# Performance work log

Hardware: AMD Instinct MI355X
Metric: run time of the kernel (lower is better)

## Reference

```python
import jax, jax.numpy as jnp
import numpy as np

B, L, D, H = 4, 2048, 1024, 16
NEG = 1e7


def pos_encodings(length, d_model, dtype):
    d_half = d_model // 2
    pos = jnp.arange(length, dtype=dtype)
    freqs = jnp.arange(d_half, dtype=dtype)
    periods = 1.0 / (10000.0 ** (freqs / d_half))
    ang = pos[:, None] * periods[None, :]          # [L, D/2]
    # interleave: even cols = sin, odd cols = cos
    return jnp.stack([jnp.sin(ang), jnp.cos(ang)], axis=-1).reshape(length, d_model)


def setup_inputs() -> dict:
    key = jax.random.key(0)
    ks = jax.random.split(key, 12)
    s = 1.0 / np.sqrt(D)
    return {
        "q": jax.random.normal(ks[0], (B, L, D), jnp.float32),
        "k": jax.random.normal(ks[1], (B, L, D), jnp.float32),
        "v": jax.random.normal(ks[2], (B, L, D), jnp.float32),
        "padding": jnp.zeros((B, L), dtype=bool),
        "Wq": jax.random.normal(ks[3], (D, D), jnp.float32) * s,
        "bq": jax.random.normal(ks[4], (D,), jnp.float32) * s,
        "Wk": jax.random.normal(ks[5], (D, D), jnp.float32) * s,
        "bk": jax.random.normal(ks[6], (D,), jnp.float32) * s,
        "Wv": jax.random.normal(ks[7], (D, D), jnp.float32) * s,
        "bv": jax.random.normal(ks[8], (D,), jnp.float32) * s,
        "Wo": jax.random.normal(ks[9], (D, D), jnp.float32) * s,
        "bo": jax.random.normal(ks[10], (D,), jnp.float32) * s,
    }


def reference(q, k, v, padding, Wq, bq, Wk, bk, Wv, bv, Wo, bo):
    dtype = q.dtype
    d_head = D // H
    pe = pos_encodings(L, D, dtype)                # cache_index = 0

    qp = (q + pe) @ Wq + bq                        # [B, L, D]
    kp = (k + pe) @ Wk + bk
    vp = v @ Wv + bv

    # ... l (h d) -> ... h l d
    def split_heads(x):
        return x.reshape(B, L, H, d_head).transpose(0, 2, 1, 3)

    qh, kh, vh = split_heads(qp), split_heads(kp), split_heads(vp)

    scores = jnp.einsum('bhqd,bhkd->bhqk', qh, kh) * (d_head ** -0.5)

    causal = jnp.triu(jnp.ones((L, L), dtype=bool), k=1)       # [L, L]
    mask = padding[:, None, None, :] | causal                  # [B, 1, L, L]
    scores = scores - mask.astype(scores.dtype) * NEG

    out = jnp.einsum('bhqk,bhkd->bhqd', jax.nn.softmax(scores, axis=-1), vh)
    out = out.transpose(0, 2, 1, 3).reshape(B, L, D)           # ... h l d -> ... l (h d)
    return out @ Wo + bo
```

## Files before the change

### kernel.cpp

```cpp
#include <hip/hip_runtime.h>
#include <hip/hip_bf16.h>


typedef __bf16 bf16_t;
typedef bf16_t bf16x8 __attribute__((ext_vector_type(8)));
typedef bf16_t bf16x4 __attribute__((ext_vector_type(4)));
typedef float  f32x4  __attribute__((ext_vector_type(4)));

#define MFMA_16x16x32(a, b, c) __builtin_amdgcn_mfma_f32_16x16x32_bf16((a), (b), (c), 0, 0, 0)

constexpr int Lc = 2048, Dc = 1024;
constexpr int Mc = 8192;
#define QSCALE 0.18033688011112042f

__device__ __forceinline__ void gload16(const void* g, void* l) {
  __builtin_amdgcn_global_load_lds(
      (const __attribute__((address_space(1))) void*)g,
      (__attribute__((address_space(3))) void*)l, 16, 0, 0);
}

template <bool DO_V>
__global__ __launch_bounds__(256)
void qkv_prep_kernel(const float* __restrict__ q, const float* __restrict__ k,
                     const float* __restrict__ v, bf16_t* __restrict__ Aq,
                     bf16_t* __restrict__ Ak, bf16_t* __restrict__ Av) {
  int id  = blockIdx.x * 256 + threadIdx.x;
  int row = id >> 7;
  int c   = (id & 127) * 8;
  int pos = row & (Lc - 1);
  float period = __expf(-(float)(c >> 1) * 0.017988946039015984f);
  const float ratio = 0.98217189f;
  float pe8[8];
#pragma unroll
  for (int j = 0; j < 4; ++j) {
    float rev = ((float)pos * period) * 0.15915494309189535f;
    float rf = rev - floorf(rev);
    pe8[2 * j]     = __builtin_amdgcn_sinf(rf);
    pe8[2 * j + 1] = __builtin_amdgcn_cosf(rf);
    period *= ratio;
  }
  size_t off = (size_t)row * Dc + c;
  f32x4 q0 = *(const f32x4*)&q[off], q1 = *(const f32x4*)&q[off + 4];
  f32x4 k0 = *(const f32x4*)&k[off], k1 = *(const f32x4*)&k[off + 4];
  bf16x8 aq, ak;
#pragma unroll
  for (int e = 0; e < 4; ++e) {
    aq[e]     = (bf16_t)(q0[e] + pe8[e]);
    aq[4 + e] = (bf16_t)(q1[e] + pe8[4 + e]);
    ak[e]     = (bf16_t)(k0[e] + pe8[e]);
    ak[4 + e] = (bf16_t)(k1[e] + pe8[4 + e]);
  }
  *(bf16x8*)&Aq[off] = aq;
  *(bf16x8*)&Ak[off] = ak;
  if (DO_V) {
    f32x4 v0 = *(const f32x4*)&v[off], v1 = *(const f32x4*)&v[off + 4];
    bf16x8 av;
#pragma unroll
    for (int e = 0; e < 4; ++e) { av[e] = (bf16_t)v0[e]; av[4 + e] = (bf16_t)v1[e]; }
    *(bf16x8*)&Av[off] = av;
  }
}

__device__ __forceinline__ void w_prep_body(const float* W, bf16_t* Wt, int tid, int blk) {
  __shared__ float tile[64][65];
  int k0 = (blk >> 4) * 64, n0 = (blk & 15) * 64;
  int tc = tid & 63, tr = tid >> 6;
#pragma unroll
  for (int j = 0; j < 16; ++j) {
    int r = j * 4 + tr;
    tile[r][tc] = W[(size_t)(k0 + r) * Dc + n0 + tc];
  }
  __syncthreads();
#pragma unroll
  for (int j = 0; j < 16; ++j) {
    int r = j * 4 + tr;
    Wt[(size_t)(n0 + r) * Dc + k0 + tc] = (bf16_t)tile[tc][r];
  }
}

__global__ __launch_bounds__(256)
void w_prep_kernel(const float* __restrict__ W, bf16_t* __restrict__ Wt) {
  w_prep_body(W, Wt, threadIdx.x, blockIdx.x);
}

__global__ __launch_bounds__(256)
void w_prep4_kernel(const float* __restrict__ W0, const float* __restrict__ W1,
                    const float* __restrict__ W2, const float* __restrict__ W3,
                    bf16_t* __restrict__ Wt) {
  int sel = blockIdx.x >> 8;
  const float* W = (sel == 0) ? W0 : (sel == 1) ? W1 : (sel == 2) ? W2 : W3;
  w_prep_body(W, Wt + (size_t)sel * Dc * Dc, threadIdx.x, blockIdx.x & 255);
}

template <bool TRANSOUT, typename OutT, int SEGS>
__global__ __launch_bounds__(512, 4)
void gemm_db_kernel(const bf16_t* __restrict__ A0, const bf16_t* __restrict__ A1,
                    const bf16_t* __restrict__ W0, const bf16_t* __restrict__ W1,
                    const float* __restrict__ b0, const float* __restrict__ b1,
                    OutT* __restrict__ C0, OutT* __restrict__ C1,
                    float s0, float s1) {
  constexpr int K = 1024, N = 1024, LDS_T = 136;
  __shared__ bf16_t smem[32768];
  int bid = blockIdx.x;
  int seg = (SEGS == 2) ? (bid >> 9) : 0;
  bid &= 511;
  const bf16_t* A    = seg ? A1 : A0;
  const bf16_t* Wt   = seg ? W1 : W0;
  const float*  bias = seg ? b1 : b0;
  OutT*         C    = seg ? C1 : C0;
  float scale        = seg ? s1 : s0;
  int xcd = bid & 7, slot = bid >> 3;
  int m0 = (xcd * 8 + (slot >> 3)) * 128;
  int n0 = (slot & 7) * 128;
  int t = threadIdx.x, lane = t & 63, w = t >> 6;
  int l16 = lane & 15, lq = lane >> 4;
  int wm = (w >> 1) * 32, wn = (w & 1) * 64;
  int srow = lane >> 3;
  int scol = ((lane & 7) ^ srow) << 3;
  int swz = l16 & 7;
  f32x4 acc[2][4] = {};

  auto STAGE = [&](int c, int k0) {
    bf16_t* Ash = &smem[c * 16384];
    bf16_t* Bsh = Ash + 8192;
#pragma unroll
    for (int j = 0; j < 2; ++j) {
      int r8 = (w * 2 + j) * 8;
      gload16(&A[(size_t)(m0 + r8 + srow) * K + k0 + scol], &Ash[r8 * 64]);
      gload16(&Wt[(size_t)(n0 + r8 + srow) * K + k0 + scol], &Bsh[r8 * 64]);
    }
  };

  STAGE(0, 0);
  int c = 0;
#pragma unroll 1
  for (int ti = 0; ti < 16; ++ti) {
    if (ti < 15) {
      STAGE(c ^ 1, (ti + 1) * 64);
      asm volatile("s_waitcnt vmcnt(4)" ::: "memory");
    } else {
      asm volatile("s_waitcnt vmcnt(0)" ::: "memory");
    }
    __builtin_amdgcn_s_barrier();
    const bf16_t* Ash = &smem[c * 16384];
    const bf16_t* Bsh = Ash + 8192;
#pragma unroll
    for (int ks = 0; ks < 2; ++ks) {
      bf16x8 af[2], bfr[4];
#pragma unroll
      for (int mt = 0; mt < 2; ++mt)
        af[mt] = *(const bf16x8*)&Ash[(wm + mt * 16 + l16) * 64 + (((ks * 4 + lq) ^ swz) << 3)];
#pragma unroll
      for (int nt = 0; nt < 4; ++nt)
        bfr[nt] = *(const bf16x8*)&Bsh[(wn + nt * 16 + l16) * 64 + (((ks * 4 + lq) ^ swz) << 3)];
#pragma unroll
      for (int mt = 0; mt < 2; ++mt)
#pragma unroll
        for (int nt = 0; nt < 4; ++nt)
          acc[mt][nt] = MFMA_16x16x32(af[mt], bfr[nt], acc[mt][nt]);
    }
    __builtin_amdgcn_s_barrier();
    c ^= 1;
  }

  if (TRANSOUT) {
    bf16_t* sT = smem;
#pragma unroll
    for (int nt = 0; nt < 4; ++nt) {
      float bv = bias[n0 + wn + nt * 16 + l16];
#pragma unroll
      for (int mt = 0; mt < 2; ++mt) {
        bf16x4 p4;
#pragma unroll
        for (int r = 0; r < 4; ++r) p4[r] = (bf16_t)(acc[mt][nt][r] + bv);
        *(bf16x4*)&sT[(wn + nt * 16 + l16) * LDS_T + wm + mt * 16 + lq * 4] = p4;
      }
    }
    __syncthreads();
    int b = m0 >> 11, kp0 = m0 & (Lc - 1);
#pragma unroll
    for (int i = 0; i < 4; ++i) {
      int cidx = t + i * 512;
      int coln = cidx >> 4, cc = (cidx & 15) * 8;
      *(bf16x8*)&((bf16_t*)C)[((size_t)b * 1024 + n0 + coln) * (size_t)Lc + kp0 + cc] =
          *(const bf16x8*)&sT[coln * LDS_T + cc];
    }
  } else {
#pragma unroll
    for (int nt = 0; nt < 4; ++nt) {
      float bv = bias[n0 + wn + nt * 16 + l16];
#pragma unroll
      for (int mt = 0; mt < 2; ++mt) {
        int row = m0 + wm + mt * 16 + lq * 4;
        int col = n0 + wn + nt * 16 + l16;
#pragma unroll
        for (int r = 0; r < 4; ++r)
          C[(size_t)(row + r) * N + col] = (OutT)((acc[mt][nt][r] + bv) * scale);
      }
    }
  }
}

__global__ __launch_bounds__(512, 4)
void gemm_af32_kernel(const float* __restrict__ A, const bf16_t* __restrict__ Wt,
                      const float* __restrict__ bias, bf16_t* __restrict__ C) {
  constexpr int K = 1024, LDS_T = 136;
  __shared__ bf16_t smem[17408];
  bf16_t* Ash = smem;
  bf16_t* Bsh = smem + 8192;
  int bid = blockIdx.x;
  int xcd = bid & 7, slot = bid >> 3;
  int m0 = (xcd * 8 + (slot >> 3)) * 128;
  int n0 = (slot & 7) * 128;
  int t = threadIdx.x, lane = t & 63, w = t >> 6;
  int l16 = lane & 15, lq = lane >> 4;
  int wm = (w >> 1) * 32, wn = (w & 1) * 64;
  int srow = lane >> 3;
  int scol = ((lane & 7) ^ srow) << 3;
  int swz = l16 & 7;
  f32x4 acc[2][4] = {};

  for (int k0 = 0; k0 < K; k0 += 64) {
#pragma unroll
    for (int i = 0; i < 2; ++i) {
      int id = t + i * 512;
      int row = id >> 3, cc = (id & 7) * 8;
      f32x4 a0 = *(const f32x4*)&A[(size_t)(m0 + row) * K + k0 + cc];
      f32x4 a1 = *(const f32x4*)&A[(size_t)(m0 + row) * K + k0 + cc + 4];
      bf16x8 ah;
#pragma unroll
      for (int e = 0; e < 4; ++e) { ah[e] = (bf16_t)a0[e]; ah[4 + e] = (bf16_t)a1[e]; }
      *(bf16x8*)&Ash[row * 64 + (((cc >> 3) ^ (row & 7)) << 3)] = ah;
    }
#pragma unroll
    for (int j = 0; j < 2; ++j) {
      int r8 = (w * 2 + j) * 8;
      gload16(&Wt[(size_t)(n0 + r8 + srow) * K + k0 + scol], &Bsh[r8 * 64]);
    }
    __syncthreads();
#pragma unroll
    for (int ks = 0; ks < 2; ++ks) {
      bf16x8 af[2], bfr[4];
#pragma unroll
      for (int mt = 0; mt < 2; ++mt)
        af[mt] = *(const bf16x8*)&Ash[(wm + mt * 16 + l16) * 64 + (((ks * 4 + lq) ^ swz) << 3)];
#pragma unroll
      for (int nt = 0; nt < 4; ++nt)
        bfr[nt] = *(const bf16x8*)&Bsh[(wn + nt * 16 + l16) * 64 + (((ks * 4 + lq) ^ swz) << 3)];
#pragma unroll
      for (int mt = 0; mt < 2; ++mt)
#pragma unroll
        for (int nt = 0; nt < 4; ++nt)
          acc[mt][nt] = MFMA_16x16x32(af[mt], bfr[nt], acc[mt][nt]);
    }
    __syncthreads();
  }

  bf16_t* sT = smem;
#pragma unroll
  for (int nt = 0; nt < 4; ++nt) {
    float bv = bias[n0 + wn + nt * 16 + l16];
#pragma unroll
    for (int mt = 0; mt < 2; ++mt) {
      bf16x4 p4;
#pragma unroll
      for (int r = 0; r < 4; ++r) p4[r] = (bf16_t)(acc[mt][nt][r] + bv);
      *(bf16x4*)&sT[(wn + nt * 16 + l16) * LDS_T + wm + mt * 16 + lq * 4] = p4;
    }
  }
  __syncthreads();
  int b = m0 >> 11, kp0 = m0 & (Lc - 1);
#pragma unroll
  for (int i = 0; i < 4; ++i) {
    int cidx = t + i * 512;
    int coln = cidx >> 4, cc = (cidx & 15) * 8;
    *(bf16x8*)&C[((size_t)b * 1024 + n0 + coln) * (size_t)Lc + kp0 + cc] =
        *(const bf16x8*)&sT[coln * LDS_T + cc];
  }
}

__global__ __launch_bounds__(256, 4)
void attn_kernel(const bf16_t* __restrict__ Qp, const bf16_t* __restrict__ Kp,
                 const bf16_t* __restrict__ VpT, bf16_t* __restrict__ O) {
  constexpr int LDP = 72;
  __shared__ bf16_t Ks[64 * 64];
  __shared__ bf16_t Vt[64 * 64];
  __shared__ bf16_t Ps[64 * LDP];
  int bid = blockIdx.x;
  int xcd = bid & 7, slot = bid >> 3;
  int bh = xcd * 8 + (slot >> 4);
  int px = slot & 15;
  int b = bh >> 4, h = bh & 15;
  int t = threadIdx.x, lane = t & 63, w = t >> 6;
  int l16 = lane & 15, lq = lane >> 4;
  int srow = lane >> 3;
  int scol = ((lane & 7) ^ srow) << 3;
  int swz = l16 & 7;
  const size_t base  = ((size_t)b * Lc) * Dc + h * 64;
  const size_t vbase = ((size_t)b * 1024 + h * 64) * (size_t)Lc;

  bf16x8 ones;
#pragma unroll
  for (int e = 0; e < 8; ++e) ones[e] = (bf16_t)1.0f;

#pragma unroll 1
  for (int phase = 0; phase < 2; ++phase) {
    int qt = phase ? 31 - px : px;
    int q0 = qt * 64;

    bf16x8 aq[2];
#pragma unroll
    for (int kd = 0; kd < 2; ++kd)
      aq[kd] = *(const bf16x8*)&Qp[base + (size_t)(q0 + w * 16 + l16) * Dc + kd * 32 + lq * 8];

    f32x4 oacc[4] = {};
    f32x4 lacc = {};
    int qrow = q0 + w * 16 + l16;

#pragma unroll 1
    for (int kt = 0; kt <= qt; ++kt) {
      int kbase = kt * 64;
#pragma unroll
      for (int j = 0; j < 2; ++j) {
        int r8 = (w * 2 + j) * 8;
        int row = r8 + srow;
        gload16(&Kp[base + (size_t)(kbase + row) * Dc + scol], &Ks[r8 * 64]);
        gload16(&VpT[vbase + (size_t)row * Lc + kbase + scol], &Vt[r8 * 64]);
      }
      __syncthreads();

      f32x4 sacc[4] = {};
#pragma unroll
      for (int ks = 0; ks < 2; ++ks) {
        bf16x8 bk[4];
#pragma unroll
        for (int nt = 0; nt < 4; ++nt)
          bk[nt] = *(const bf16x8*)&Ks[(nt * 16 + l16) * 64 + (((ks * 4 + lq) ^ swz) << 3)];
#pragma unroll
        for (int nt = 0; nt < 4; ++nt)
          sacc[nt] = MFMA_16x16x32(bk[nt], aq[ks], sacc[nt]);
      }

      if (kt == qt) {
#pragma unroll
        for (int nt = 0; nt < 4; ++nt)
#pragma unroll
          for (int r = 0; r < 4; ++r)
            if (kbase + nt * 16 + lq * 4 + r > qrow) sacc[nt][r] = -1.0e7f;
      }

#pragma unroll
      for (int nt = 0; nt < 4; ++nt) {
        bf16x4 p4;
#pragma unroll
        for (int r = 0; r < 4; ++r) p4[r] = (bf16_t)exp2f(sacc[nt][r]);
        *(bf16x4*)&Ps[(w * 16 + l16) * LDP + nt * 16 + lq * 4] = p4;
      }

#pragma unroll
      for (int ks = 0; ks < 2; ++ks) {
        bf16x8 ap = *(const bf16x8*)&Ps[(w * 16 + l16) * LDP + ks * 32 + lq * 8];
        lacc = MFMA_16x16x32(ap, ones, lacc);
        bf16x8 bv[4];
#pragma unroll
        for (int nt = 0; nt < 4; ++nt)
          bv[nt] = *(const bf16x8*)&Vt[(nt * 16 + l16) * 64 + (((ks * 4 + lq) ^ swz) << 3)];
#pragma unroll
        for (int nt = 0; nt < 4; ++nt)
          oacc[nt] = MFMA_16x16x32(ap, bv[nt], oacc[nt]);
      }
      __syncthreads();
    }

#pragma unroll
    for (int r = 0; r < 4; ++r) {
      float inv = __builtin_amdgcn_rcpf(lacc[r]);
      int row = q0 + w * 16 + lq * 4 + r;
#pragma unroll
      for (int nt = 0; nt < 4; ++nt)
        O[base + (size_t)row * Dc + nt * 16 + l16] = (bf16_t)(oacc[nt][r] * inv);
    }
  }
}

extern "C" void kernel_launch(void* const* d_in, const int* in_sizes, int n_in,
                              void* d_out, int out_size, void* d_ws, size_t ws_size,
                              hipStream_t stream) {
  (void)in_sizes; (void)n_in; (void)out_size;
  const float* q  = (const float*)d_in[0];
  const float* k  = (const float*)d_in[1];
  const float* v  = (const float*)d_in[2];
  const float* Wq = (const float*)d_in[4];
  const float* bq = (const float*)d_in[5];
  const float* Wk = (const float*)d_in[6];
  const float* bk = (const float*)d_in[7];
  const float* Wv = (const float*)d_in[8];
  const float* bv = (const float*)d_in[9];
  const float* Wo = (const float*)d_in[10];
  const float* bo = (const float*)d_in[11];
  float* out = (float*)d_out;

  char* ws = (char*)d_ws;
  constexpr size_t WT_B  = (size_t)Dc * Dc * 2;
  constexpr size_t MAT_B = (size_t)Mc * Dc * 2;
  constexpr size_t WSZ   = (size_t)Dc * Dc;

  if (ws_size >= 4 * WT_B + 5 * MAT_B) {
    bf16_t* WT  = (bf16_t*)(ws);
    bf16_t* Aq  = (bf16_t*)(ws + 4 * WT_B);
    bf16_t* Ak  = (bf16_t*)(ws + 4 * WT_B + 1 * MAT_B);
    bf16_t* Av  = (bf16_t*)(ws + 4 * WT_B + 2 * MAT_B);
    bf16_t* Qp  = (bf16_t*)(ws + 4 * WT_B + 3 * MAT_B);
    bf16_t* Kp  = (bf16_t*)(ws + 4 * WT_B + 4 * MAT_B);
    bf16_t* VpT = Aq;
    bf16_t* Ob  = Qp;

    qkv_prep_kernel<true><<<4096, 256, 0, stream>>>(q, k, v, Aq, Ak, Av);
    w_prep4_kernel<<<1024, 256, 0, stream>>>(Wq, Wk, Wv, Wo, WT);
    gemm_db_kernel<false, bf16_t, 2><<<1024, 512, 0, stream>>>(
        Aq, Ak, WT, WT + WSZ, bq, bk, Qp, Kp, QSCALE, 1.0f);
    gemm_db_kernel<true, bf16_t, 1><<<512, 512, 0, stream>>>(
        Av, Av, WT + 2 * WSZ, WT + 2 * WSZ, bv, bv, VpT, VpT, 1.0f, 1.0f);
    attn_kernel<<<1024, 256, 0, stream>>>(Qp, Kp, VpT, Ob);
    gemm_db_kernel<false, float, 1><<<512, 512, 0, stream>>>(
        Ob, Ob, WT + 3 * WSZ, WT + 3 * WSZ, bo, bo, out, out, 1.0f, 1.0f);
  } else {
    bf16_t* WT  = (bf16_t*)(ws);
    bf16_t* Aq  = (bf16_t*)(ws + WT_B);
    bf16_t* Ak  = (bf16_t*)(ws + WT_B + 1 * MAT_B);
    bf16_t* Qp  = (bf16_t*)(ws + WT_B + 2 * MAT_B);
    bf16_t* Kp  = Aq;
    bf16_t* VpT = Ak;
    bf16_t* Ob  = Qp;

    qkv_prep_kernel<false><<<4096, 256, 0, stream>>>(q, k, nullptr, Aq, Ak, nullptr);

    w_prep_kernel<<<256, 256, 0, stream>>>(Wq, WT);
    gemm_db_kernel<false, bf16_t, 1><<<512, 512, 0, stream>>>(
        Aq, Aq, WT, WT, bq, bq, Qp, Qp, QSCALE, QSCALE);

    w_prep_kernel<<<256, 256, 0, stream>>>(Wk, WT);
    gemm_db_kernel<false, bf16_t, 1><<<512, 512, 0, stream>>>(
        Ak, Ak, WT, WT, bk, bk, Kp, Kp, 1.0f, 1.0f);

    w_prep_kernel<<<256, 256, 0, stream>>>(Wv, WT);
    gemm_af32_kernel<<<512, 512, 0, stream>>>(v, WT, bv, VpT);

    attn_kernel<<<1024, 256, 0, stream>>>(Qp, Kp, VpT, Ob);

    w_prep_kernel<<<256, 256, 0, stream>>>(Wo, WT);
    gemm_db_kernel<false, float, 1><<<512, 512, 0, stream>>>(
        Ob, Ob, WT, WT, bo, bo, out, out, 1.0f, 1.0f);
  }
}
```

Baseline: 314.3 us.

## Double-buffer K/V tiles in attention and fuse QKV projections into one launch

The attention kernel now double-buffers its K and V LDS tiles. It prefetches the next key tile with async global-to-LDS loads before computing on the current one, using a partial vmcnt wait and raw barriers in place of __syncthreads. The P tile is stored with an XOR swizzle instead of padding, which keeps LDS use near the occupancy budget. A new workspace path with a separate VpT buffer runs the Q, K and V projections as one 1536-block GEMM launch, transposing only the V segment. The attention change adds LDS footprint per block, and the new launch path needs more workspace.

```diff
diff --git a/kernel.cpp b/kernel.cpp
--- a/kernel.cpp
+++ b/kernel.cpp
@@ -92,23 +92,28 @@
   w_prep_body(W, Wt + (size_t)sel * Dc * Dc, threadIdx.x, blockIdx.x & 255);
 }
 
-template <bool TRANSOUT, typename OutT, int SEGS>
+template <int TMODE, typename OutT, int SEGS>
 __global__ __launch_bounds__(512, 4)
 void gemm_db_kernel(const bf16_t* __restrict__ A0, const bf16_t* __restrict__ A1,
+                    const bf16_t* __restrict__ A2,
                     const bf16_t* __restrict__ W0, const bf16_t* __restrict__ W1,
+                    const bf16_t* __restrict__ W2,
                     const float* __restrict__ b0, const float* __restrict__ b1,
+                    const float* __restrict__ b2,
                     OutT* __restrict__ C0, OutT* __restrict__ C1,
-                    float s0, float s1) {
+                    OutT* __restrict__ C2,
+                    float s0, float s1, float s2) {
   constexpr int K = 1024, N = 1024, LDS_T = 136;
   __shared__ bf16_t smem[32768];
   int bid = blockIdx.x;
-  int seg = (SEGS == 2) ? (bid >> 9) : 0;
+  int seg = (SEGS >= 2) ? (bid >> 9) : 0;
   bid &= 511;
-  const bf16_t* A    = seg ? A1 : A0;
-  const bf16_t* Wt   = seg ? W1 : W0;
-  const float*  bias = seg ? b1 : b0;
-  OutT*         C    = seg ? C1 : C0;
-  float scale        = seg ? s1 : s0;
+  const bf16_t* A    = (seg == 0) ? A0 : (seg == 1) ? A1 : A2;
+  const bf16_t* Wt   = (seg == 0) ? W0 : (seg == 1) ? W1 : W2;
+  const float*  bias = (seg == 0) ? b0 : (seg == 1) ? b1 : b2;
+  OutT*         C    = (seg == 0) ? C0 : (seg == 1) ? C1 : C2;
+  float scale        = (seg == 0) ? s0 : (seg == 1) ? s1 : s2;
+  bool dotrans       = (TMODE == 1) || (TMODE == 2 && seg == 2);
   int xcd = bid & 7, slot = bid >> 3;
   int m0 = (xcd * 8 + (slot >> 3)) * 128;
   int n0 = (slot & 7) * 128;
@@ -163,7 +168,7 @@
     c ^= 1;
   }
 
-  if (TRANSOUT) {
+  if (dotrans) {
     bf16_t* sT = smem;
 #pragma unroll
     for (int nt = 0; nt < 4; ++nt) {
@@ -282,10 +287,9 @@
 __global__ __launch_bounds__(256, 4)
 void attn_kernel(const bf16_t* __restrict__ Qp, const bf16_t* __restrict__ Kp,
                  const bf16_t* __restrict__ VpT, bf16_t* __restrict__ O) {
-  constexpr int LDP = 72;
-  __shared__ bf16_t Ks[64 * 64];
-  __shared__ bf16_t Vt[64 * 64];
-  __shared__ bf16_t Ps[64 * LDP];
+  __shared__ bf16_t Ks[2][4096];
+  __shared__ bf16_t Vt[2][4096];
+  __shared__ bf16_t Ps[4096];
   int bid = blockIdx.x;
   int xcd = bid & 7, slot = bid >> 3;
   int bh = xcd * 8 + (slot >> 4);
@@ -303,6 +307,17 @@
 #pragma unroll
   for (int e = 0; e < 8; ++e) ones[e] = (bf16_t)1.0f;
 
+  auto STAGE = [&](int cc, int kt) {
+    int kbase = kt * 64;
+#pragma unroll
+    for (int j = 0; j < 2; ++j) {
+      int r8 = (w * 2 + j) * 8;
+      int row = r8 + srow;
+      gload16(&Kp[base + (size_t)(kbase + row) * Dc + scol], &Ks[cc][r8 * 64]);
+      gload16(&VpT[vbase + (size_t)row * Lc + kbase + scol], &Vt[cc][r8 * 64]);
+    }
+  };
+
 #pragma unroll 1
   for (int phase = 0; phase < 2; ++phase) {
     int qt = phase ? 31 - px : px;
@@ -317,25 +332,26 @@
     f32x4 lacc = {};
     int qrow = q0 + w * 16 + l16;
 
+    STAGE(0, 0);
+    int c = 0;
 #pragma unroll 1
     for (int kt = 0; kt <= qt; ++kt) {
+      if (kt < qt) {
+        STAGE(c ^ 1, kt + 1);
+        asm volatile("s_waitcnt vmcnt(4)" ::: "memory");
+      } else {
+        asm volatile("s_waitcnt vmcnt(0)" ::: "memory");
+      }
+      __builtin_amdgcn_s_barrier();
+
       int kbase = kt * 64;
-#pragma unroll
-      for (int j = 0; j < 2; ++j) {
-        int r8 = (w * 2 + j) * 8;
-        int row = r8 + srow;
-        gload16(&Kp[base + (size_t)(kbase + row) * Dc + scol], &Ks[r8 * 64]);
-        gload16(&VpT[vbase + (size_t)row * Lc + kbase + scol], &Vt[r8 * 64]);
-      }
-      __syncthreads();
-
       f32x4 sacc[4] = {};
 #pragma unroll
       for (int ks = 0; ks < 2; ++ks) {
         bf16x8 bk[4];
 #pragma unroll
         for (int nt = 0; nt < 4; ++nt)
-          bk[nt] = *(const bf16x8*)&Ks[(nt * 16 + l16) * 64 + (((ks * 4 + lq) ^ swz) << 3)];
+          bk[nt] = *(const bf16x8*)&Ks[c][(nt * 16 + l16) * 64 + (((ks * 4 + lq) ^ swz) << 3)];
 #pragma unroll
         for (int nt = 0; nt < 4; ++nt)
           sacc[nt] = MFMA_16x16x32(bk[nt], aq[ks], sacc[nt]);
@@ -354,22 +370,24 @@
         bf16x4 p4;
 #pragma unroll
         for (int r = 0; r < 4; ++r) p4[r] = (bf16_t)exp2f(sacc[nt][r]);
-        *(bf16x4*)&Ps[(w * 16 + l16) * LDP + nt * 16 + lq * 4] = p4;
+        int k4 = nt * 4 + lq;
+        *(bf16x4*)&Ps[(w * 16 + l16) * 64 + (((k4 >> 1) ^ swz) << 3) + ((k4 & 1) << 2)] = p4;
       }
 
 #pragma unroll
       for (int ks = 0; ks < 2; ++ks) {
-        bf16x8 ap = *(const bf16x8*)&Ps[(w * 16 + l16) * LDP + ks * 32 + lq * 8];
+        bf16x8 ap = *(const bf16x8*)&Ps[(w * 16 + l16) * 64 + (((ks * 4 + lq) ^ swz) << 3)];
         lacc = MFMA_16x16x32(ap, ones, lacc);
         bf16x8 bv[4];
 #pragma unroll
         for (int nt = 0; nt < 4; ++nt)
-          bv[nt] = *(const bf16x8*)&Vt[(nt * 16 + l16) * 64 + (((ks * 4 + lq) ^ swz) << 3)];
+          bv[nt] = *(const bf16x8*)&Vt[c][(nt * 16 + l16) * 64 + (((ks * 4 + lq) ^ swz) << 3)];
 #pragma unroll
         for (int nt = 0; nt < 4; ++nt)
           oacc[nt] = MFMA_16x16x32(ap, bv[nt], oacc[nt]);
       }
-      __syncthreads();
+      __builtin_amdgcn_s_barrier();
+      c ^= 1;
     }
 
 #pragma unroll
@@ -405,7 +423,26 @@
   constexpr size_t MAT_B = (size_t)Mc * Dc * 2;
   constexpr size_t WSZ   = (size_t)Dc * Dc;
 
-  if (ws_size >= 4 * WT_B + 5 * MAT_B) {
+  if (ws_size >= 4 * WT_B + 6 * MAT_B) {
+    bf16_t* WT  = (bf16_t*)(ws);
+    bf16_t* Aq  = (bf16_t*)(ws + 4 * WT_B);
+    bf16_t* Ak  = (bf16_t*)(ws + 4 * WT_B + 1 * MAT_B);
+    bf16_t* Av  = (bf16_t*)(ws + 4 * WT_B + 2 * MAT_B);
+    bf16_t* Qp  = (bf16_t*)(ws + 4 * WT_B + 3 * MAT_B);
+    bf16_t* Kp  = (bf16_t*)(ws + 4 * WT_B + 4 * MAT_B);
+    bf16_t* VpT = (bf16_t*)(ws + 4 * WT_B + 5 * MAT_B);
+    bf16_t* Ob  = Qp;
+
+    qkv_prep_kernel<true><<<4096, 256, 0, stream>>>(q, k, v, Aq, Ak, Av);
+    w_prep4_kernel<<<1024, 256, 0, stream>>>(Wq, Wk, Wv, Wo, WT);
+    gemm_db_kernel<2, bf16_t, 3><<<1536, 512, 0, stream>>>(
+        Aq, Ak, Av, WT, WT + WSZ, WT + 2 * WSZ, bq, bk, bv,
+        Qp, Kp, VpT, QSCALE, 1.0f, 1.0f);
+    attn_kernel<<<1024, 256, 0, stream>>>(Qp, Kp, VpT, Ob);
+    gemm_db_kernel<0, float, 1><<<512, 512, 0, stream>>>(
+        Ob, Ob, Ob, WT + 3 * WSZ, WT + 3 * WSZ, WT + 3 * WSZ, bo, bo, bo,
+        out, out, out, 1.0f, 1.0f, 1.0f);
+  } else if (ws_size >= 4 * WT_B + 5 * MAT_B) {
     bf16_t* WT  = (bf16_t*)(ws);
     bf16_t* Aq  = (bf16_t*)(ws + 4 * WT_B);
     bf16_t* Ak  = (bf16_t*)(ws + 4 * WT_B + 1 * MAT_B);
@@ -417,13 +454,16 @@
 
     qkv_prep_kernel<true><<<4096, 256, 0, stream>>>(q, k, v, Aq, Ak, Av);
     w_prep4_kernel<<<1024, 256, 0, stream>>>(Wq, Wk, Wv, Wo, WT);
-    gemm_db_kernel<false, bf16_t, 2><<<1024, 512, 0, stream>>>(
-        Aq, Ak, WT, WT + WSZ, bq, bk, Qp, Kp, QSCALE, 1.0f);
-    gemm_db_kernel<true, bf16_t, 1><<<512, 512, 0, stream>>>(
-        Av, Av, WT + 2 * WSZ, WT + 2 * WSZ, bv, bv, VpT, VpT, 1.0f, 1.0f);
+    gemm_db_kernel<0, bf16_t, 2><<<1024, 512, 0, stream>>>(
+        Aq, Ak, Ak, WT, WT + WSZ, WT + WSZ, bq, bk, bk,
+        Qp, Kp, Kp, QSCALE, 1.0f, 1.0f);
+    gemm_db_kernel<1, bf16_t, 1><<<512, 512, 0, stream>>>(
+        Av, Av, Av, WT + 2 * WSZ, WT + 2 * WSZ, WT + 2 * WSZ, bv, bv, bv,
+        VpT, VpT, VpT, 1.0f, 1.0f, 1.0f);
     attn_kernel<<<1024, 256, 0, stream>>>(Qp, Kp, VpT, Ob);
-    gemm_db_kernel<false, float, 1><<<512, 512, 0, stream>>>(
-        Ob, Ob, WT + 3 * WSZ, WT + 3 * WSZ, bo, bo, out, out, 1.0f, 1.0f);
+    gemm_db_kernel<0, float, 1><<<512, 512, 0, stream>>>(
+        Ob, Ob, Ob, WT + 3 * WSZ, WT + 3 * WSZ, WT + 3 * WSZ, bo, bo, bo,
+        out, out, out, 1.0f, 1.0f, 1.0f);
   } else {
     bf16_t* WT  = (bf16_t*)(ws);
     bf16_t* Aq  = (bf16_t*)(ws + WT_B);
@@ -436,12 +476,12 @@
     qkv_prep_kernel<false><<<4096, 256, 0, stream>>>(q, k, nullptr, Aq, Ak, nullptr);
 
     w_prep_kernel<<<256, 256, 0, stream>>>(Wq, WT);
-    gemm_db_kernel<false, bf16_t, 1><<<512, 512, 0, stream>>>(
-        Aq, Aq, WT, WT, bq, bq, Qp, Qp, QSCALE, QSCALE);
+    gemm_db_kernel<0, bf16_t, 1><<<512, 512, 0, stream>>>(
+        Aq, Aq, Aq, WT, WT, WT, bq, bq, bq, Qp, Qp, Qp, QSCALE, QSCALE, QSCALE);
 
     w_prep_kernel<<<256, 256, 0, stream>>>(Wk, WT);
-    gemm_db_kernel<false, bf16_t, 1><<<512, 512, 0, stream>>>(
-        Ak, Ak, WT, WT, bk, bk, Kp, Kp, 1.0f, 1.0f);
+    gemm_db_kernel<0, bf16_t, 1><<<512, 512, 0, stream>>>(
+        Ak, Ak, Ak, WT, WT, WT, bk, bk, bk, Kp, Kp, Kp, 1.0f, 1.0f, 1.0f);
 
     w_prep_kernel<<<256, 256, 0, stream>>>(Wv, WT);
     gemm_af32_kernel<<<512, 512, 0, stream>>>(v, WT, bv, VpT);
@@ -449,7 +489,7 @@
     attn_kernel<<<1024, 256, 0, stream>>>(Qp, Kp, VpT, Ob);
 
     w_prep_kernel<<<256, 256, 0, stream>>>(Wo, WT);
-    gemm_db_kernel<false, float, 1><<<512, 512, 0, stream>>>(
-        Ob, Ob, WT, WT, bo, bo, out, out, 1.0f, 1.0f);
-  }
-}
+    gemm_db_kernel<0, float, 1><<<512, 512, 0, stream>>>(
+        Ob, Ob, Ob, WT, WT, WT, bo, bo, bo, out, out, out, 1.0f, 1.0f, 1.0f);
+  }
+}
```

Result: no change. 312.0 us (-0.7%).

## Fuse whole attention pipeline into one cooperative persistent kernel with grid syncs

Applied to the files above, without the earlier changes.

Adds a cooperative mega-kernel of 512 blocks of 512 threads that runs input/weight prep, the Q/K/V projections, attention and the output projection in sequence, separated by grid-wide syncs. The aim is to remove multiple kernel launches and the gaps between them. It also fuses the prep kernels and the QKV GEMMs into single launches for the fallback path. The risk is that the persistent grid (about 2 blocks per CU) has lower occupancy than the separate launches, that grid.sync adds cost, and that the attention phase's load balance changes. If cooperative launch fails, the code falls back to the fused multi-kernel path.

```diff
diff --git a/kernel.cpp b/kernel.cpp
--- a/kernel.cpp
+++ b/kernel.cpp
@@ -1,5 +1,8 @@
 #include <hip/hip_runtime.h>
 #include <hip/hip_bf16.h>
+#include <hip/hip_cooperative_groups.h>
+
+namespace cg = cooperative_groups;
 
 
 typedef __bf16 bf16_t;
@@ -11,6 +14,7 @@
 
 constexpr int Lc = 2048, Dc = 1024;
 constexpr int Mc = 8192;
+constexpr size_t WSZ_E = (size_t)Dc * Dc;
 #define QSCALE 0.18033688011112042f
 
 __device__ __forceinline__ void gload16(const void* g, void* l) {
@@ -20,11 +24,9 @@
 }
 
 template <bool DO_V>
-__global__ __launch_bounds__(256)
-void qkv_prep_kernel(const float* __restrict__ q, const float* __restrict__ k,
-                     const float* __restrict__ v, bf16_t* __restrict__ Aq,
-                     bf16_t* __restrict__ Ak, bf16_t* __restrict__ Av) {
-  int id  = blockIdx.x * 256 + threadIdx.x;
+__device__ __forceinline__ void qkv_prep_body(
+    const float* q, const float* k, const float* v,
+    bf16_t* Aq, bf16_t* Ak, bf16_t* Av, int id) {
   int row = id >> 7;
   int c   = (id & 127) * 8;
   int pos = row & (Lc - 1);
@@ -61,58 +63,65 @@
   }
 }
 
-__device__ __forceinline__ void w_prep_body(const float* W, bf16_t* Wt, int tid, int blk) {
-  __shared__ float tile[64][65];
+template <bool DO_V>
+__global__ __launch_bounds__(256)
+void qkv_prep_kernel(const float* __restrict__ q, const float* __restrict__ k,
+                     const float* __restrict__ v, bf16_t* __restrict__ Aq,
+                     bf16_t* __restrict__ Ak, bf16_t* __restrict__ Av) {
+  qkv_prep_body<DO_V>(q, k, v, Aq, Ak, Av, blockIdx.x * 256 + threadIdx.x);
+}
+
+__device__ __forceinline__ void w_prep_body(const float* W, bf16_t* Wt, int tid,
+                                            int blk, float* tile) {
   int k0 = (blk >> 4) * 64, n0 = (blk & 15) * 64;
   int tc = tid & 63, tr = tid >> 6;
 #pragma unroll
   for (int j = 0; j < 16; ++j) {
     int r = j * 4 + tr;
-    tile[r][tc] = W[(size_t)(k0 + r) * Dc + n0 + tc];
+    tile[r * 65 + tc] = W[(size_t)(k0 + r) * Dc + n0 + tc];
   }
   __syncthreads();
 #pragma unroll
   for (int j = 0; j < 16; ++j) {
     int r = j * 4 + tr;
-    Wt[(size_t)(n0 + r) * Dc + k0 + tc] = (bf16_t)tile[tc][r];
+    Wt[(size_t)(n0 + r) * Dc + k0 + tc] = (bf16_t)tile[tc * 65 + r];
   }
 }
 
 __global__ __launch_bounds__(256)
 void w_prep_kernel(const float* __restrict__ W, bf16_t* __restrict__ Wt) {
-  w_prep_body(W, Wt, threadIdx.x, blockIdx.x);
+  __shared__ float tile[4160];
+  w_prep_body(W, Wt, threadIdx.x, blockIdx.x, tile);
 }
 
 __global__ __launch_bounds__(256)
-void w_prep4_kernel(const float* __restrict__ W0, const float* __restrict__ W1,
-                    const float* __restrict__ W2, const float* __restrict__ W3,
-                    bf16_t* __restrict__ Wt) {
-  int sel = blockIdx.x >> 8;
-  const float* W = (sel == 0) ? W0 : (sel == 1) ? W1 : (sel == 2) ? W2 : W3;
-  w_prep_body(W, Wt + (size_t)sel * Dc * Dc, threadIdx.x, blockIdx.x & 255);
-}
-
-template <bool TRANSOUT, typename OutT, int SEGS>
-__global__ __launch_bounds__(512, 4)
-void gemm_db_kernel(const bf16_t* __restrict__ A0, const bf16_t* __restrict__ A1,
-                    const bf16_t* __restrict__ W0, const bf16_t* __restrict__ W1,
-                    const float* __restrict__ b0, const float* __restrict__ b1,
-                    OutT* __restrict__ C0, OutT* __restrict__ C1,
-                    float s0, float s1) {
+void prep_fused_kernel(const float* __restrict__ q, const float* __restrict__ k,
+                       const float* __restrict__ v, bf16_t* __restrict__ Aq,
+                       bf16_t* __restrict__ Ak, bf16_t* __restrict__ Av,
+                       const float* __restrict__ W0, const float* __restrict__ W1,
+                       const float* __restrict__ W2, const float* __restrict__ W3,
+                       bf16_t* __restrict__ Wt) {
+  __shared__ float tile[4160];
+  if (blockIdx.x >= 4096) {
+    int bb = blockIdx.x - 4096;
+    int sel = bb >> 8;
+    const float* W = (sel == 0) ? W0 : (sel == 1) ? W1 : (sel == 2) ? W2 : W3;
+    w_prep_body(W, Wt + (size_t)sel * WSZ_E, threadIdx.x, bb & 255, tile);
+    return;
+  }
+  qkv_prep_body<true>(q, k, v, Aq, Ak, Av, blockIdx.x * 256 + threadIdx.x);
+}
+
+template <bool TRANS, typename OutT>
+__device__ __forceinline__ void gemm_body(
+    const bf16_t* __restrict__ A, const bf16_t* __restrict__ Wt,
+    const float* __restrict__ bias, OutT* __restrict__ C, float scale,
+    int bid, int t, bf16_t* __restrict__ smem) {
   constexpr int K = 1024, N = 1024, LDS_T = 136;
-  __shared__ bf16_t smem[32768];
-  int bid = blockIdx.x;
-  int seg = (SEGS == 2) ? (bid >> 9) : 0;
-  bid &= 511;
-  const bf16_t* A    = seg ? A1 : A0;
-  const bf16_t* Wt   = seg ? W1 : W0;
-  const float*  bias = seg ? b1 : b0;
-  OutT*         C    = seg ? C1 : C0;
-  float scale        = seg ? s1 : s0;
   int xcd = bid & 7, slot = bid >> 3;
   int m0 = (xcd * 8 + (slot >> 3)) * 128;
   int n0 = (slot & 7) * 128;
-  int t = threadIdx.x, lane = t & 63, w = t >> 6;
+  int lane = t & 63, w = t >> 6;
   int l16 = lane & 15, lq = lane >> 4;
   int wm = (w >> 1) * 32, wn = (w & 1) * 64;
   int srow = lane >> 3;
@@ -163,7 +172,7 @@
     c ^= 1;
   }
 
-  if (TRANSOUT) {
+  if (TRANS) {
     bf16_t* sT = smem;
 #pragma unroll
     for (int nt = 0; nt < 4; ++nt) {
@@ -199,6 +208,57 @@
       }
     }
   }
+}
+
+__global__ __launch_bounds__(512, 4)
+void gemm_qkv_kernel(const bf16_t* __restrict__ Aq, const bf16_t* __restrict__ Ak,
+                     const bf16_t* __restrict__ Av, const bf16_t* __restrict__ WT,
+                     const float* __restrict__ bq, const float* __restrict__ bk,
+                     const float* __restrict__ bv, bf16_t* __restrict__ Qp,
+                     bf16_t* __restrict__ Kp, bf16_t* __restrict__ VpT) {
+  __shared__ bf16_t smem[32768];
+  int bid = blockIdx.x, seg = bid >> 9; bid &= 511;
+  if (seg == 0)
+    gemm_body<false, bf16_t>(Aq, WT, bq, Qp, QSCALE, bid, threadIdx.x, smem);
+  else if (seg == 1)
+    gemm_body<false, bf16_t>(Ak, WT + WSZ_E, bk, Kp, 1.0f, bid, threadIdx.x, smem);
+  else
+    gemm_body<true, bf16_t>(Av, WT + 2 * WSZ_E, bv, VpT, 1.0f, bid, threadIdx.x, smem);
+}
+
+__global__ __launch_bounds__(512, 4)
+void gemm_qk_kernel(const bf16_t* __restrict__ Aq, const bf16_t* __restrict__ Ak,
+                    const bf16_t* __restrict__ WT, const float* __restrict__ bq,
+                    const float* __restrict__ bk, bf16_t* __restrict__ Qp,
+                    bf16_t* __restrict__ Kp) {
+  __shared__ bf16_t smem[32768];
+  int bid = blockIdx.x, seg = bid >> 9; bid &= 511;
+  if (seg == 0)
+    gemm_body<false, bf16_t>(Aq, WT, bq, Qp, QSCALE, bid, threadIdx.x, smem);
+  else
+    gemm_body<false, bf16_t>(Ak, WT + WSZ_E, bk, Kp, 1.0f, bid, threadIdx.x, smem);
+}
+
+__global__ __launch_bounds__(512, 4)
+void gemm_v_kernel(const bf16_t* __restrict__ Av, const bf16_t* __restrict__ Wt,
+                   const float* __restrict__ bv, bf16_t* __restrict__ VpT) {
+  __shared__ bf16_t smem[32768];
+  gemm_body<true, bf16_t>(Av, Wt, bv, VpT, 1.0f, blockIdx.x, threadIdx.x, smem);
+}
+
+__global__ __launch_bounds__(512, 4)
+void gemm_bf_kernel(const bf16_t* __restrict__ A, const bf16_t* __restrict__ Wt,
+                    const float* __restrict__ bias, bf16_t* __restrict__ C,
+                    float scale) {
+  __shared__ bf16_t smem[32768];
+  gemm_body<false, bf16_t>(A, Wt, bias, C, scale, blockIdx.x, threadIdx.x, smem);
+}
+
+__global__ __launch_bounds__(512, 4)
+void gemm_o_kernel(const bf16_t* __restrict__ A, const bf16_t* __restrict__ Wt,
+                   const float* __restrict__ bias, float* __restrict__ C) {
+  __shared__ bf16_t smem[32768];
+  gemm_body<false, float>(A, Wt, bias, C, 1.0f, blockIdx.x, threadIdx.x, smem);
 }
 
 __global__ __launch_bounds__(512, 4)
@@ -279,19 +339,16 @@
   }
 }
 
-__global__ __launch_bounds__(256, 4)
-void attn_kernel(const bf16_t* __restrict__ Qp, const bf16_t* __restrict__ Kp,
-                 const bf16_t* __restrict__ VpT, bf16_t* __restrict__ O) {
+__device__ __forceinline__ void attn_body(
+    const bf16_t* __restrict__ Qp, const bf16_t* __restrict__ Kp,
+    const bf16_t* __restrict__ VpT, bf16_t* __restrict__ O,
+    int bh, int px, int tid, bf16_t* __restrict__ alds) {
   constexpr int LDP = 72;
-  __shared__ bf16_t Ks[64 * 64];
-  __shared__ bf16_t Vt[64 * 64];
-  __shared__ bf16_t Ps[64 * LDP];
-  int bid = blockIdx.x;
-  int xcd = bid & 7, slot = bid >> 3;
-  int bh = xcd * 8 + (slot >> 4);
-  int px = slot & 15;
+  bf16_t* Ks = alds;
+  bf16_t* Vt = alds + 4096;
+  bf16_t* Ps = alds + 8192;
   int b = bh >> 4, h = bh & 15;
-  int t = threadIdx.x, lane = t & 63, w = t >> 6;
+  int lane = tid & 63, w = tid >> 6;
   int l16 = lane & 15, lq = lane >> 4;
   int srow = lane >> 3;
   int scol = ((lane & 7) ^ srow) << 3;
@@ -361,13 +418,13 @@
       for (int ks = 0; ks < 2; ++ks) {
         bf16x8 ap = *(const bf16x8*)&Ps[(w * 16 + l16) * LDP + ks * 32 + lq * 8];
         lacc = MFMA_16x16x32(ap, ones, lacc);
-        bf16x8 bv[4];
-#pragma unroll
-        for (int nt = 0; nt < 4; ++nt)
-          bv[nt] = *(const bf16x8*)&Vt[(nt * 16 + l16) * 64 + (((ks * 4 + lq) ^ swz) << 3)];
-#pragma unroll
-        for (int nt = 0; nt < 4; ++nt)
-          oacc[nt] = MFMA_16x16x32(ap, bv[nt], oacc[nt]);
+        bf16x8 bv2[4];
+#pragma unroll
+        for (int nt = 0; nt < 4; ++nt)
+          bv2[nt] = *(const bf16x8*)&Vt[(nt * 16 + l16) * 64 + (((ks * 4 + lq) ^ swz) << 3)];
+#pragma unroll
+        for (int nt = 0; nt < 4; ++nt)
+          oacc[nt] = MFMA_16x16x32(ap, bv2[nt], oacc[nt]);
       }
       __syncthreads();
     }
@@ -381,6 +438,69 @@
         O[base + (size_t)row * Dc + nt * 16 + l16] = (bf16_t)(oacc[nt][r] * inv);
     }
   }
+}
+
+__global__ __launch_bounds__(256, 4)
+void attn_kernel(const bf16_t* __restrict__ Qp, const bf16_t* __restrict__ Kp,
+                 const bf16_t* __restrict__ VpT, bf16_t* __restrict__ O) {
+  __shared__ bf16_t alds[12800];
+  int bid = blockIdx.x;
+  int xcd = bid & 7, slot = bid >> 3;
+  int bh = xcd * 8 + (slot >> 4);
+  int px = slot & 15;
+  attn_body(Qp, Kp, VpT, O, bh, px, threadIdx.x, alds);
+}
+
+__global__ __launch_bounds__(512, 4)
+void mega_kernel(const float* __restrict__ q, const float* __restrict__ k,
+                 const float* __restrict__ v,
+                 const float* __restrict__ Wq, const float* __restrict__ bq,
+                 const float* __restrict__ Wk, const float* __restrict__ bk,
+                 const float* __restrict__ Wv, const float* __restrict__ bv,
+                 const float* __restrict__ Wo, const float* __restrict__ bo,
+                 bf16_t* __restrict__ Aq, bf16_t* __restrict__ Ak,
+                 bf16_t* __restrict__ Av, bf16_t* __restrict__ WT,
+                 bf16_t* __restrict__ Qp, bf16_t* __restrict__ Kp,
+                 bf16_t* __restrict__ VpT, float* __restrict__ out) {
+  __shared__ __align__(16) char msmem[65536];
+  cg::grid_group grid = cg::this_grid();
+  int phys = blockIdx.x;
+  int t = threadIdx.x;
+
+  {
+    int gtid = phys * 512 + t;
+#pragma unroll 1
+    for (int it = 0; it < 4; ++it)
+      qkv_prep_body<true>(q, k, v, Aq, Ak, Av, gtid + it * 262144);
+    int grp = t >> 8;
+    int lg = phys * 2 + grp;
+    int sel = lg >> 8;
+    const float* W = (sel == 0) ? Wq : (sel == 1) ? Wk : (sel == 2) ? Wv : Wo;
+    w_prep_body(W, WT + (size_t)sel * WSZ_E, t & 255, lg & 255,
+                (float*)(msmem + grp * 16640));
+  }
+  __threadfence();
+  grid.sync();
+
+  gemm_body<false, bf16_t>(Aq, WT,            bq, Qp,  QSCALE, phys, t, (bf16_t*)msmem);
+  __syncthreads();
+  gemm_body<false, bf16_t>(Ak, WT + WSZ_E,    bk, Kp,  1.0f,   phys, t, (bf16_t*)msmem);
+  __syncthreads();
+  gemm_body<true,  bf16_t>(Av, WT + 2 * WSZ_E, bv, VpT, 1.0f,  phys, t, (bf16_t*)msmem);
+  __threadfence();
+  grid.sync();
+
+  {
+    int grp = t >> 8, t256 = t & 255;
+    int xcd = phys & 7, r = phys >> 3;
+    int px = r & 15, bp = r >> 4;
+    int bh = xcd * 8 + bp * 2 + grp;
+    attn_body(Qp, Kp, VpT, Qp, bh, px, t256, (bf16_t*)(msmem + grp * 25600));
+  }
+  __threadfence();
+  grid.sync();
+
+  gemm_body<false, float>(Qp, WT + 3 * WSZ_E, bo, out, 1.0f, phys, t, (bf16_t*)msmem);
 }
 
 extern "C" void kernel_launch(void* const* d_in, const int* in_sizes, int n_in,
@@ -403,9 +523,30 @@
   char* ws = (char*)d_ws;
   constexpr size_t WT_B  = (size_t)Dc * Dc * 2;
   constexpr size_t MAT_B = (size_t)Mc * Dc * 2;
-  constexpr size_t WSZ   = (size_t)Dc * Dc;
-
-  if (ws_size >= 4 * WT_B + 5 * MAT_B) {
+
+  if (ws_size >= 4 * WT_B + 6 * MAT_B) {
+    bf16_t* WT  = (bf16_t*)(ws);
+    bf16_t* Aq  = (bf16_t*)(ws + 4 * WT_B);
+    bf16_t* Ak  = (bf16_t*)(ws + 4 * WT_B + 1 * MAT_B);
+    bf16_t* Av  = (bf16_t*)(ws + 4 * WT_B + 2 * MAT_B);
+    bf16_t* Qp  = (bf16_t*)(ws + 4 * WT_B + 3 * MAT_B);
+    bf16_t* Kp  = (bf16_t*)(ws + 4 * WT_B + 4 * MAT_B);
+    bf16_t* VpT = (bf16_t*)(ws + 4 * WT_B + 5 * MAT_B);
+
+    void* args[] = {&q, &k, &v, &Wq, &bq, &Wk, &bk, &Wv, &bv, &Wo, &bo,
+                    &Aq, &Ak, &Av, &WT, &Qp, &Kp, &VpT, &out};
+    hipError_t err = hipLaunchCooperativeKernel(
+        (const void*)mega_kernel, dim3(512), dim3(512), args, 0u, stream);
+    if (err == hipSuccess) return;
+    (void)hipGetLastError();
+
+    prep_fused_kernel<<<5120, 256, 0, stream>>>(q, k, v, Aq, Ak, Av,
+                                                Wq, Wk, Wv, Wo, WT);
+    gemm_qkv_kernel<<<1536, 512, 0, stream>>>(Aq, Ak, Av, WT, bq, bk, bv,
+                                              Qp, Kp, VpT);
+    attn_kernel<<<1024, 256, 0, stream>>>(Qp, Kp, VpT, Qp);
+    gemm_o_kernel<<<512, 512, 0, stream>>>(Qp, WT + 3 * WSZ_E, bo, out);
+  } else if (ws_size >= 4 * WT_B + 5 * MAT_B) {
     bf16_t* WT  = (bf16_t*)(ws);
     bf16_t* Aq  = (bf16_t*)(ws + 4 * WT_B);
     bf16_t* Ak  = (bf16_t*)(ws + 4 * WT_B + 1 * MAT_B);
@@ -413,17 +554,13 @@
     bf16_t* Qp  = (bf16_t*)(ws + 4 * WT_B + 3 * MAT_B);
     bf16_t* Kp  = (bf16_t*)(ws + 4 * WT_B + 4 * MAT_B);
     bf16_t* VpT = Aq;
-    bf16_t* Ob  = Qp;
-
-    qkv_prep_kernel<true><<<4096, 256, 0, stream>>>(q, k, v, Aq, Ak, Av);
-    w_prep4_kernel<<<1024, 256, 0, stream>>>(Wq, Wk, Wv, Wo, WT);
-    gemm_db_kernel<false, bf16_t, 2><<<1024, 512, 0, stream>>>(
-        Aq, Ak, WT, WT + WSZ, bq, bk, Qp, Kp, QSCALE, 1.0f);
-    gemm_db_kernel<true, bf16_t, 1><<<512, 512, 0, stream>>>(
-        Av, Av, WT + 2 * WSZ, WT + 2 * WSZ, bv, bv, VpT, VpT, 1.0f, 1.0f);
-    attn_kernel<<<1024, 256, 0, stream>>>(Qp, Kp, VpT, Ob);
-    gemm_db_kernel<false, float, 1><<<512, 512, 0, stream>>>(
-        Ob, Ob, WT + 3 * WSZ, WT + 3 * WSZ, bo, bo, out, out, 1.0f, 1.0f);
+
+    prep_fused_kernel<<<5120, 256, 0, stream>>>(q, k, v, Aq, Ak, Av,
+                                                Wq, Wk, Wv, Wo, WT);
+    gemm_qk_kernel<<<1024, 512, 0, stream>>>(Aq, Ak, WT, bq, bk, Qp, Kp);
+    gemm_v_kernel<<<512, 512, 0, stream>>>(Av, WT + 2 * WSZ_E, bv, VpT);
+    attn_kernel<<<1024, 256, 0, stream>>>(Qp, Kp, VpT, Qp);
+    gemm_o_kernel<<<512, 512, 0, stream>>>(Qp, WT + 3 * WSZ_E, bo, out);
   } else {
     bf16_t* WT  = (bf16_t*)(ws);
     bf16_t* Aq  = (bf16_t*)(ws + WT_B);
@@ -431,25 +568,16 @@
     bf16_t* Qp  = (bf16_t*)(ws + WT_B + 2 * MAT_B);
     bf16_t* Kp  = Aq;
     bf16_t* VpT = Ak;
-    bf16_t* Ob  = Qp;
 
     qkv_prep_kernel<false><<<4096, 256, 0, stream>>>(q, k, nullptr, Aq, Ak, nullptr);
-
     w_prep_kernel<<<256, 256, 0, stream>>>(Wq, WT);
-    gemm_db_kernel<false, bf16_t, 1><<<512, 512, 0, stream>>>(
-        Aq, Aq, WT, WT, bq, bq, Qp, Qp, QSCALE, QSCALE);
-
+    gemm_bf_kernel<<<512, 512, 0, stream>>>(Aq, WT, bq, Qp, QSCALE);
     w_prep_kernel<<<256, 256, 0, stream>>>(Wk, WT);
-    gemm_db_kernel<false, bf16_t, 1><<<512, 512, 0, stream>>>(
-        Ak, Ak, WT, WT, bk, bk, Kp, Kp, 1.0f, 1.0f);
-
+    gemm_bf_kernel<<<512, 512, 0, stream>>>(Ak, WT, bk, Kp, 1.0f);
     w_prep_kernel<<<256, 256, 0, stream>>>(Wv, WT);
     gemm_af32_kernel<<<512, 512, 0, stream>>>(v, WT, bv, VpT);
-
-    attn_kernel<<<1024, 256, 0, stream>>>(Qp, Kp, VpT, Ob);
-
+    attn_kernel<<<1024, 256, 0, stream>>>(Qp, Kp, VpT, Qp);
     w_prep_kernel<<<256, 256, 0, stream>>>(Wo, WT);
-    gemm_db_kernel<false, float, 1><<<512, 512, 0, stream>>>(
-        Ob, Ob, WT, WT, bo, bo, out, out, 1.0f, 1.0f);
-  }
-}
+    gemm_o_kernel<<<512, 512, 0, stream>>>(Qp, WT, bo, out);
+  }
+}
```

Result: slower. 853.0 us (+171.4%).
